# Performance work log

Hardware: AMD Instinct MI355X
Metric: run time of the kernel (lower is better)

## Reference

```python
import jax, jax.numpy as jnp
import numpy as np

IMG, P, C = 224, 16, 3
D, H, MLP = 512, 8, 2048
L, NCLS = 10, 10      # budget, classes
N = (IMG // P) ** 2   # 196 patches
PD = C * P * P        # patch_dim = 768


def setup_inputs() -> dict:
    key = jax.random.key(0)
    ks = jax.random.split(key, 32)
    w = lambda k, shape: (jax.random.normal(k, shape, jnp.float32) * 0.02)
    return {
        'x': jax.random.normal(ks[0], (32, C, IMG, IMG), jnp.float32),
        'y': jax.random.randint(ks[1], (32, 1), 0, NCLS),
        'pos_emb': w(ks[2], (1, N + 1, D)),
        'cls_tok': w(ks[3], (1, 1, D)),
        'Wp': w(ks[4], (D, PD)), 'bp': jnp.zeros((D,), jnp.float32),
        'Wqkv': w(ks[5], (3 * D, D)),
        'Wo': w(ks[6], (D, D)), 'bo': jnp.zeros((D,), jnp.float32),
        'ln1_g': jnp.ones((D,), jnp.float32), 'ln1_b': jnp.zeros((D,), jnp.float32),
        'ln2_g': jnp.ones((D,), jnp.float32), 'ln2_b': jnp.zeros((D,), jnp.float32),
        'W1': w(ks[7], (MLP, D)), 'b1': jnp.zeros((MLP,), jnp.float32),
        'W2': w(ks[8], (D, MLP)), 'b2': jnp.zeros((D,), jnp.float32),
        'lnh_g': jnp.ones((D,), jnp.float32), 'lnh_b': jnp.zeros((D,), jnp.float32),
        'Wh1': w(ks[9], (MLP, D)), 'bh1': jnp.zeros((MLP,), jnp.float32),
        'Wh2': w(ks[10], (1, MLP)), 'bh2': jnp.zeros((1,), jnp.float32),
        'lnc_g': jnp.ones((D,), jnp.float32), 'lnc_b': jnp.zeros((D,), jnp.float32),
        'Wc1': w(ks[11], (MLP, D)), 'bc1': jnp.zeros((MLP,), jnp.float32),
        'Wc2': w(ks[12], (NCLS, MLP)), 'bc2': jnp.zeros((NCLS,), jnp.float32),
    }


def _ln(u, g, b):
    mu = u.mean(-1, keepdims=True)
    v = ((u - mu) ** 2).mean(-1, keepdims=True)
    return (u - mu) / jnp.sqrt(v + 1e-5) * g + b


def _gelu(u):
    return jax.nn.gelu(u, approximate=False)


def reference(x, y, pos_emb, cls_tok, Wp, bp, Wqkv, Wo, bo,
              ln1_g, ln1_b, ln2_g, ln2_b, W1, b1, W2, b2,
              lnh_g, lnh_b, Wh1, bh1, Wh2, bh2,
              lnc_g, lnc_b, Wc1, bc1, Wc2, bc2):
    b = x.shape[0]
    hp = IMG // P
    # patchify: b c (h p1) (w p2) -> b (h w) (p1 p2 c)
    xp = x.reshape(b, C, hp, P, hp, P).transpose(0, 2, 4, 3, 5, 1).reshape(b, N, PD)
    e = xp @ Wp.T + bp                                   # [b, N, D]
    z = jnp.concatenate([jnp.broadcast_to(cls_tok, (b, 1, D)), e], 1) + pos_emb[:, :N + 1]

    scale = D ** -0.5

    def attn(u):
        q, k, v = jnp.split(u @ Wqkv.T, 3, axis=-1)
        hsplit = lambda t: t.reshape(b, -1, H, D // H).transpose(0, 2, 1, 3)  # b h n d
        q, k, v = hsplit(q), hsplit(k), hsplit(v)
        a = jax.nn.softmax(jnp.einsum('bhid,bhjd->bhij', q, k) * scale, axis=-1)
        o = jnp.einsum('bhij,bhjd->bhid', a, v).transpose(0, 2, 1, 3).reshape(b, -1, D)
        return o @ Wo.T + bo

    def ff(u):
        return _gelu(u @ W1.T + b1) @ W2.T + b2

    def halt(u):
        h = _gelu(_ln(u, lnh_g, lnh_b) @ Wh1.T + bh1) @ Wh2.T + bh2  # [b, n, 1]
        return jax.nn.sigmoid(h).mean(1)[:, 0]                        # [b]

    def step(u, _):
        u = u + attn(_ln(u, ln1_g, ln1_b))
        u = u + ff(_ln(u, ln2_g, ln2_b))
        return u, (u[:, 0], halt(u))

    _, (cls_outs, halts) = jax.lax.scan(step, z, None, length=L)
    cls_outs = cls_outs.transpose(1, 0, 2)   # [b, L, D]
    halts = halts.T                          # [b, L]

    logits = _gelu(_ln(cls_outs, lnc_g, lnc_b) @ Wc1.T + bc1) @ Wc2.T + bc2  # [b, L, 10]
    logp = jax.nn.log_softmax(logits, -1)
    lab = y[:, 0]
    ce = -jnp.take_along_axis(logp, jnp.broadcast_to(lab[:, None, None], (b, L, 1)), axis=2)[..., 0]  # [b, L]

    idx = jnp.argmin(ce, axis=1) + 1                     # [b], halting step per sample
    steps = jnp.arange(L)
    mask = (steps[None, :] < idx[:, None]).astype(ce.dtype)
    denom = idx.astype(ce.dtype)
    ref_ce = (ce * mask).sum(1) / denom                  # per-sample mean over first idx steps

    # halt labels: 1 for steps < idx-1, 0 at step idx-1 (only first idx entries count)
    hl = jnp.where(steps[None, :] == (idx[:, None] - 1), 0.0, 1.0)
    p = jnp.clip(halts, 1e-7, 1.0 - 1e-7)
    bce = -(hl * jnp.log(p) + (1.0 - hl) * jnp.log1p(-p))
    halt_loss = (bce * mask).sum(1) / denom

    return ref_ce.mean() + halt_loss.mean()
```

## Files before the change

### kernel.cpp

```cpp
#include <hip/hip_runtime.h>
#include <math.h>

#define BBATCH 32
#define NTOK 197
#define NPATCH 196
#define PDIM 768
#define DDIM 512
#define NHEAD 8
#define DHEAD 64
#define MLPDIM 2048
#define NLAYER 10
#define NCLASS 10
#define MTOK (BBATCH*NTOK)
#define MPAD 6400
#define MPATCH (BBATCH*NPATCH)
#define QKVROWS (MTOK + 16)

typedef unsigned short u16;
typedef __attribute__((ext_vector_type(8))) short bf16x8;
typedef __attribute__((ext_vector_type(4))) float f32x4;
typedef __attribute__((ext_vector_type(8))) unsigned short ushort8;

__device__ __forceinline__ float gelu_f(float x) {
    return 0.5f * x * (1.0f + erff(x * 0.70710678118654752440f));
}
__device__ __forceinline__ float bf2f(u16 u) {
    union { unsigned int i; float f; } v; v.i = ((unsigned int)u) << 16; return v.f;
}
__device__ __forceinline__ u16 f2bf(float f) {
    union { float f; unsigned int u; } v; v.f = f;
    unsigned int r = v.u + 0x7FFFu + ((v.u >> 16) & 1u);
    return (u16)(r >> 16);
}
__device__ __forceinline__ void gload_lds16(const u16* g, u16* l) {
    __builtin_amdgcn_global_load_lds((const __attribute__((address_space(1))) void*)g,
                                     (__attribute__((address_space(3))) void*)l, 16, 0, 0);
}

template<int ACT, int HASB, int HASR, int OUTBF, int HALT>
__global__ __launch_bounds__(256)
void mgemm_kernel(const u16* __restrict__ A, const u16* __restrict__ W,
                  const float* __restrict__ bias, const float* __restrict__ res,
                  void* __restrict__ Cout, int M, int Nn, int K)
{
    __shared__ u16 As[2][128 * 64];
    __shared__ u16 Bs[2][128 * 64];
    const int tid = threadIdx.x;
    const int lane = tid & 63;
    const int wid = tid >> 6;
    const int wr = wid >> 1, wc = wid & 1;

    const int gx = gridDim.x;
    const int nwg = gx * gridDim.y;
    const int wg = blockIdx.y * gx + blockIdx.x;
    const int q = nwg >> 3, r = nwg & 7;
    const int xcd = wg & 7, idx = wg >> 3;
    const int swz = (xcd < r) ? xcd * (q + 1) + idx
                              : r * (q + 1) + (xcd - r) * q + idx;
    const int m0 = (swz / gx) * 128, n0 = (swz % gx) * 128;

    f32x4 acc[4][4] = {};

    const int srow = tid >> 3;
    const int dcb  = (tid & 7) << 4;

    auto stage = [&](int buf, int k0) {
        #pragma unroll
        for (int p = 0; p < 4; ++p) {
            int rr = p * 32 + srow;
            int scb = dcb ^ ((rr & 7) << 4);
            gload_lds16(A + (size_t)(m0 + rr) * K + k0 + (scb >> 1), &As[buf][p * 2048 + tid * 8]);
            gload_lds16(W + (size_t)(n0 + rr) * K + k0 + (scb >> 1), &Bs[buf][p * 2048 + tid * 8]);
        }
    };
    auto compute = [&](int buf) {
        #pragma unroll
        for (int kk = 0; kk < 64; kk += 32) {
            const int kb = (kk + ((lane >> 4) << 3)) << 1;
            bf16x8 af[4], bfr[4];
            #pragma unroll
            for (int mi = 0; mi < 4; ++mi) {
                int ar = wr * 64 + mi * 16 + (lane & 15);
                af[mi] = *(const bf16x8*)&As[buf][ar * 64 + ((kb ^ ((ar & 7) << 4)) >> 1)];
            }
            #pragma unroll
            for (int ni = 0; ni < 4; ++ni) {
                int br = wc * 64 + ni * 16 + (lane & 15);
                bfr[ni] = *(const bf16x8*)&Bs[buf][br * 64 + ((kb ^ ((br & 7) << 4)) >> 1)];
            }
            #pragma unroll
            for (int mi = 0; mi < 4; ++mi)
                #pragma unroll
                for (int ni = 0; ni < 4; ++ni)
                    acc[mi][ni] = __builtin_amdgcn_mfma_f32_16x16x32_bf16(
                        af[mi], bfr[ni], acc[mi][ni], 0, 0, 0);
        }
    };

    const int NT = K >> 6;
    stage(0, 0);
    int cur = 0;
    #pragma unroll 1
    for (int t = 0; t < NT - 1; ++t) {
        stage(cur ^ 1, (t + 1) << 6);
        asm volatile("s_waitcnt vmcnt(8)" ::: "memory");
        __builtin_amdgcn_s_barrier();
        compute(cur);
        __builtin_amdgcn_s_barrier();
        cur ^= 1;
    }
    asm volatile("s_waitcnt vmcnt(0)" ::: "memory");
    __builtin_amdgcn_s_barrier();
    compute(cur);

    if (HALT) {
        const float* Wh2v = res;
        float* hout = (float*)Cout;
        #pragma unroll
        for (int mi = 0; mi < 4; ++mi) {
            #pragma unroll
            for (int j = 0; j < 4; ++j) {
                int row = m0 + wr * 64 + mi * 16 + ((lane >> 4) << 2) + j;
                float part = 0.0f;
                #pragma unroll
                for (int ni = 0; ni < 4; ++ni) {
                    int col = n0 + wc * 64 + ni * 16 + (lane & 15);
                    float v = gelu_f(acc[mi][ni][j] + bias[col]);
                    part += v * Wh2v[col];
                }
                #pragma unroll
                for (int off = 1; off < 16; off <<= 1) part += __shfl_xor(part, off, 64);
                if ((lane & 15) == 0 && row < M) atomicAdd(&hout[row], part);
            }
        }
        return;
    }

    float* outf = (float*)Cout;
    u16*   outb = (u16*)Cout;
    #pragma unroll
    for (int mi = 0; mi < 4; ++mi) {
        #pragma unroll
        for (int j = 0; j < 4; ++j) {
            int row = m0 + wr * 64 + mi * 16 + ((lane >> 4) << 2) + j;
            if (row >= M) continue;
            #pragma unroll
            for (int ni = 0; ni < 4; ++ni) {
                int col = n0 + wc * 64 + ni * 16 + (lane & 15);
                float v = acc[mi][ni][j];
                if (HASB) v += bias[col];
                if (ACT)  v = gelu_f(v);
                if (HASR) v += res[(size_t)row * Nn + col];
                if (OUTBF) outb[(size_t)row * Nn + col] = f2bf(v);
                else       outf[(size_t)row * Nn + col] = v;
            }
        }
    }
}

__global__ __launch_bounds__(256)
void f2bf_kernel(const float* __restrict__ in, u16* __restrict__ out, int n4)
{
    int i = blockIdx.x * 256 + threadIdx.x;
    if (i >= n4) return;
    float4 v = ((const float4*)in)[i];
    u16 o0 = f2bf(v.x), o1 = f2bf(v.y), o2 = f2bf(v.z), o3 = f2bf(v.w);
    out[i * 4 + 0] = o0; out[i * 4 + 1] = o1; out[i * 4 + 2] = o2; out[i * 4 + 3] = o3;
}

__global__ __launch_bounds__(256)
void ln_kernel(const float* __restrict__ X, const float* __restrict__ g,
               const float* __restrict__ bb, u16* __restrict__ Y, int M)
{
    int wave = (blockIdx.x * 4) + (threadIdx.x >> 6);
    int lane = threadIdx.x & 63;
    if (wave >= M) return;
    const float* x = X + (size_t)wave * DDIM;
    float v[8];
    float s = 0.0f;
    #pragma unroll
    for (int i = 0; i < 8; i++) { v[i] = x[lane + i * 64]; s += v[i]; }
    #pragma unroll
    for (int off = 32; off; off >>= 1) s += __shfl_xor(s, off, 64);
    float mu = s * (1.0f / 512.0f);
    float q = 0.0f;
    #pragma unroll
    for (int i = 0; i < 8; i++) { float d = v[i] - mu; q += d * d; }
    #pragma unroll
    for (int off = 32; off; off >>= 1) q += __shfl_xor(q, off, 64);
    float inv = 1.0f / sqrtf(q * (1.0f / 512.0f) + 1e-5f);
    u16* y = Y + (size_t)wave * DDIM;
    #pragma unroll
    for (int i = 0; i < 8; i++) {
        int c = lane + i * 64;
        y[c] = f2bf((v[i] - mu) * inv * g[c] + bb[c]);
    }
}

__global__ __launch_bounds__(256)
void patch_kernel(const float* __restrict__ x, u16* __restrict__ xp)
{
    size_t idx = (size_t)blockIdx.x * 256 + threadIdx.x;
    if (idx >= (size_t)MPATCH * PDIM) return;
    int pd = (int)(idx % PDIM);
    int bn = (int)(idx / PDIM);
    int n = bn % NPATCH, b = bn / NPATCH;
    int c = pd % 3, pix = pd / 3;
    int px = pix % 16, py = pix / 16;
    int hx = n % 14, hy = n / 14;
    int row = hy * 16 + py, col = hx * 16 + px;
    xp[idx] = f2bf(x[((size_t)(b * 3 + c) * 224 + row) * 224 + col]);
}

__global__ __launch_bounds__(256)
void assemble_kernel(const float* __restrict__ e, const float* __restrict__ clstok,
                     const float* __restrict__ pos, float* __restrict__ U)
{
    size_t idx = (size_t)blockIdx.x * 256 + threadIdx.x;
    if (idx >= (size_t)MTOK * DDIM) return;
    int d = (int)(idx % DDIM);
    int bt = (int)(idx / DDIM);
    int t = bt % NTOK, b = bt / NTOK;
    float v = (t == 0) ? clstok[d] : e[((size_t)b * NPATCH + (t - 1)) * DDIM + d];
    U[idx] = v + pos[t * DDIM + d];
}

__global__ __launch_bounds__(256)
void attn_mfma_kernel(const u16* __restrict__ qkv, u16* __restrict__ O)
{
    __shared__ u16 Ks[208 * 64];
    __shared__ u16 Vt[64 * 208];
    __shared__ u16 Pl[4 * 16 * 208];

    const int bh = blockIdx.x >> 1;
    const int half = blockIdx.x & 1;
    const int b = bh >> 3, h = bh & 7;
    const int tid = threadIdx.x;
    const int lane = tid & 63, wid = tid >> 6;
    const size_t base = ((size_t)b * NTOK) * 1536 + (size_t)h * 64;

    {
        int j0 = tid >> 3;
        int d0 = (tid & 7) * 8;
        for (int p = 0; p < 7; ++p) {
            int j = p * 32 + j0;
            if (j < 208) {
                bf16x8 v = {};
                if (j < NTOK) v = *(const bf16x8*)&qkv[base + (size_t)j * 1536 + 512 + d0];
                int byt = (j * 128 + d0 * 2) ^ ((j & 7) << 4);
                *(bf16x8*)((char*)Ks + byt) = v;
            }
        }
    }
    {
        int d = tid & 63;
        int jg = tid >> 6;
        for (int j = jg * 52; j < jg * 52 + 52; ++j) {
            u16 v = (j < NTOK) ? qkv[base + (size_t)j * 1536 + 1024 + d] : (u16)0;
            int byt = (d * 416 + j * 2) ^ ((d & 7) << 4);
            *(u16*)((char*)Vt + byt) = v;
        }
    }
    __syncthreads();

    u16* Pw = Pl + wid * 16 * 208;
    const float scale = 0.04419417382415922f;
    const int t0   = half ? 7 : 0;
    const int tcnt = half ? 6 : 7;
    const int g = lane >> 4;
    const int mycol = lane & 15;

    for (int ti = wid; ti < tcnt; ti += 4) {
        const int r0 = (t0 + ti) * 16;
        bf16x8 qf[2];
        #pragma unroll
        for (int ks = 0; ks < 2; ++ks) {
            int row = r0 + mycol;
            int col = ks * 32 + (g << 3);
            qf[ks] = *(const bf16x8*)&qkv[base + (size_t)row * 1536 + col];
        }
        f32x4 s[13];
        #pragma unroll
        for (int ct = 0; ct < 13; ++ct) s[ct] = (f32x4){0.f, 0.f, 0.f, 0.f};
        #pragma unroll
        for (int ks = 0; ks < 2; ++ks) {
            int kbyte = (ks * 32 + (g << 3)) * 2;
            #pragma unroll
            for (int ct = 0; ct < 13; ++ct) {
                int n = ct * 16 + mycol;
                bf16x8 kf = *(const bf16x8*)((char*)Ks + ((n * 128 + kbyte) ^ ((n & 7) << 4)));
                s[ct] = __builtin_amdgcn_mfma_f32_16x16x32_bf16(qf[ks], kf, s[ct], 0, 0, 0);
            }
        }
        float m[4], sum[4];
        #pragma unroll
        for (int j = 0; j < 4; ++j) m[j] = -1e30f;
        #pragma unroll
        for (int ct = 0; ct < 13; ++ct) {
            bool valid = (ct * 16 + mycol) < NTOK;
            #pragma unroll
            for (int j = 0; j < 4; ++j) {
                float v = valid ? s[ct][j] * scale : -1e30f;
                s[ct][j] = v;
                m[j] = fmaxf(m[j], v);
            }
        }
        #pragma unroll
        for (int off = 1; off < 16; off <<= 1)
            #pragma unroll
            for (int j = 0; j < 4; ++j) m[j] = fmaxf(m[j], __shfl_xor(m[j], off, 64));
        #pragma unroll
        for (int j = 0; j < 4; ++j) sum[j] = 0.0f;
        #pragma unroll
        for (int ct = 0; ct < 13; ++ct)
            #pragma unroll
            for (int j = 0; j < 4; ++j) {
                float e = expf(s[ct][j] - m[j]);
                s[ct][j] = e;
                sum[j] += e;
            }
        #pragma unroll
        for (int off = 1; off < 16; off <<= 1)
            #pragma unroll
            for (int j = 0; j < 4; ++j) sum[j] += __shfl_xor(sum[j], off, 64);
        float inv[4];
        #pragma unroll
        for (int j = 0; j < 4; ++j) inv[j] = 1.0f / sum[j];
        #pragma unroll
        for (int ct = 0; ct < 13; ++ct) {
            int col = ct * 16 + mycol;
            #pragma unroll
            for (int j = 0; j < 4; ++j) {
                int row = (g << 2) + j;
                int byt = (row * 416 + col * 2) ^ ((row & 7) << 4);
                *(u16*)((char*)Pw + byt) = f2bf(s[ct][j] * inv[j]);
            }
        }
        #pragma unroll
        for (int nt = 0; nt < 4; ++nt) {
            f32x4 o = (f32x4){0.f, 0.f, 0.f, 0.f};
            #pragma unroll
            for (int ks = 0; ks < 7; ++ks) {
                bf16x8 pf = {}, vf = {};
                bool live = !(ks == 6 && g >= 2);
                if (live) {
                    int kbyte = (ks * 32 + (g << 3)) * 2;
                    pf = *(const bf16x8*)((char*)Pw + ((mycol * 416 + kbyte) ^ ((mycol & 7) << 4)));
                    int vrow = nt * 16 + mycol;
                    vf = *(const bf16x8*)((char*)Vt + ((vrow * 416 + kbyte) ^ ((vrow & 7) << 4)));
                }
                o = __builtin_amdgcn_mfma_f32_16x16x32_bf16(pf, vf, o, 0, 0, 0);
            }
            #pragma unroll
            for (int j = 0; j < 4; ++j) {
                int grow = r0 + (g << 2) + j;
                if (grow < NTOK)
                    O[((size_t)b * NTOK + grow) * DDIM + h * 64 + nt * 16 + mycol] = f2bf(o[j]);
            }
        }
    }
}

__global__ __launch_bounds__(64)
void halt_mean_cls_kernel(const float* __restrict__ hsc, const float* __restrict__ bh2,
                          const float* __restrict__ U,
                          float* __restrict__ halts, float* __restrict__ cls, int l)
{
    int b = blockIdx.x, lane = threadIdx.x;
    float bb = bh2[0];
    float s = 0.0f;
    for (int t = lane; t < NTOK; t += 64) {
        float raw = hsc[b * NTOK + t] + bb;
        s += 1.0f / (1.0f + expf(-raw));
    }
    #pragma unroll
    for (int off = 32; off; off >>= 1) s += __shfl_xor(s, off, 64);
    if (lane == 0) halts[b * NLAYER + l] = s * (1.0f / (float)NTOK);
    for (int d = lane; d < DDIM; d += 64)
        cls[((size_t)b * NLAYER + l) * DDIM + d] = U[(size_t)b * NTOK * DDIM + d];
}

__global__ __launch_bounds__(256)
void head_logits_kernel(const u16* __restrict__ Hh, const float* __restrict__ Wc2,
                        const float* __restrict__ bc2, float* __restrict__ logits)
{
    int wave = (blockIdx.x * 4) + (threadIdx.x >> 6);
    int lane = threadIdx.x & 63;
    if (wave >= BBATCH * NLAYER) return;
    const u16* row = Hh + (size_t)wave * MLPDIM;
    float rv[32];
    #pragma unroll
    for (int i = 0; i < 32; i++) rv[i] = bf2f(row[lane + i * 64]);
    #pragma unroll
    for (int c = 0; c < NCLASS; c++) {
        float s = 0.0f;
        #pragma unroll
        for (int i = 0; i < 32; i++) s = fmaf(rv[i], Wc2[c * MLPDIM + lane + i * 64], s);
        #pragma unroll
        for (int off = 32; off; off >>= 1) s += __shfl_xor(s, off, 64);
        if (lane == 0) logits[wave * NCLASS + c] = s + bc2[c];
    }
}

__global__ __launch_bounds__(256)
void ce_kernel(const float* __restrict__ logits, const int* __restrict__ y,
               float* __restrict__ ce)
{
    int r = blockIdx.x * 256 + threadIdx.x;
    if (r >= BBATCH * NLAYER) return;
    const float* lg = logits + (size_t)r * NCLASS;
    float mx = lg[0];
    #pragma unroll
    for (int i = 1; i < NCLASS; i++) mx = fmaxf(mx, lg[i]);
    float s = 0.0f;
    #pragma unroll
    for (int i = 0; i < NCLASS; i++) s += expf(lg[i] - mx);
    int lab = y[r / NLAYER];
    ce[r] = -(lg[lab] - mx - logf(s));
}

__global__ __launch_bounds__(64)
void loss_kernel(const float* __restrict__ ce, const float* __restrict__ halts,
                 float* __restrict__ out)
{
    int b = threadIdx.x;
    float total = 0.0f;
    if (b < BBATCH) {
        const float* c = ce + b * NLAYER;
        int idx = 0; float mn = c[0];
        for (int l = 1; l < NLAYER; l++) if (c[l] < mn) { mn = c[l]; idx = l; }
        idx += 1;
        float acc = 0.0f;
        for (int l = 0; l < idx; l++) {
            acc += c[l];
            float p = halts[b * NLAYER + l];
            p = fminf(fmaxf(p, 1e-7f), 1.0f - 1e-7f);
            float hl = (l == idx - 1) ? 0.0f : 1.0f;
            acc += -(hl * logf(p) + (1.0f - hl) * log1pf(-p));
        }
        total = acc / (float)idx;
    }
    #pragma unroll
    for (int off = 32; off; off >>= 1) total += __shfl_xor(total, off, 64);
    if (threadIdx.x == 0) out[0] = total * (1.0f / (float)BBATCH);
}

extern "C" void kernel_launch(void* const* d_in, const int* in_sizes, int n_in,
                              void* d_out, int out_size, void* d_ws, size_t ws_size,
                              hipStream_t stream)
{
    const float* x      = (const float*)d_in[0];
    const int*   y      = (const int*)d_in[1];
    const float* pos    = (const float*)d_in[2];
    const float* clstok = (const float*)d_in[3];
    const float* Wp     = (const float*)d_in[4];
    const float* bp     = (const float*)d_in[5];
    const float* Wqkv   = (const float*)d_in[6];
    const float* Wo     = (const float*)d_in[7];
    const float* bo     = (const float*)d_in[8];
    const float* ln1g   = (const float*)d_in[9];
    const float* ln1b   = (const float*)d_in[10];
    const float* ln2g   = (const float*)d_in[11];
    const float* ln2b   = (const float*)d_in[12];
    const float* W1     = (const float*)d_in[13];
    const float* b1     = (const float*)d_in[14];
    const float* W2     = (const float*)d_in[15];
    const float* b2     = (const float*)d_in[16];
    const float* lnhg   = (const float*)d_in[17];
    const float* lnhb   = (const float*)d_in[18];
    const float* Wh1    = (const float*)d_in[19];
    const float* bh1    = (const float*)d_in[20];
    const float* Wh2    = (const float*)d_in[21];
    const float* bh2    = (const float*)d_in[22];
    const float* lncg   = (const float*)d_in[23];
    const float* lncb   = (const float*)d_in[24];
    const float* Wc1    = (const float*)d_in[25];
    const float* bc1    = (const float*)d_in[26];
    const float* Wc2    = (const float*)d_in[27];
    const float* bc2    = (const float*)d_in[28];

    float* U      = (float*)d_ws;
    float* EMB    = U + (size_t)MTOK * DDIM;
    float* CLS    = EMB + (size_t)MPATCH * DDIM;
    float* LOGITS = CLS + (size_t)BBATCH * NLAYER * DDIM;
    float* CE     = LOGITS + BBATCH * NLAYER * NCLASS;
    float* HSC    = CE + BBATCH * NLAYER;
    float* HALTS  = HSC + MTOK;
    u16* QKVb = (u16*)(HALTS + BBATCH * NLAYER + 32);
    u16* LNB  = QKVb + (size_t)QKVROWS * 1536;
    u16* HB   = LNB + (size_t)MPAD * DDIM;
    u16* XP   = HB + (size_t)MPAD * MLPDIM;
    u16* CLNB = XP + (size_t)MPATCH * PDIM;
    u16* wWp  = CLNB + 384 * DDIM;
    u16* wWqkv= wWp   + 512 * 768;
    u16* wWo  = wWqkv + 1536 * 512;
    u16* wW1  = wWo   + 512 * 512;
    u16* wW2  = wW1   + 2048 * 512;
    u16* wWh1 = wW2   + 512 * 2048;
    u16* wWc1 = wWh1  + 2048 * 512;

    dim3 blk(256);

    f2bf_kernel<<<dim3((512*768/4 + 255)/256), blk, 0, stream>>>(Wp, wWp, 512*768/4);
    f2bf_kernel<<<dim3((1536*512/4 + 255)/256), blk, 0, stream>>>(Wqkv, wWqkv, 1536*512/4);
    f2bf_kernel<<<dim3((512*512/4 + 255)/256), blk, 0, stream>>>(Wo, wWo, 512*512/4);
    f2bf_kernel<<<dim3((2048*512/4 + 255)/256), blk, 0, stream>>>(W1, wW1, 2048*512/4);
    f2bf_kernel<<<dim3((512*2048/4 + 255)/256), blk, 0, stream>>>(W2, wW2, 512*2048/4);
    f2bf_kernel<<<dim3((2048*512/4 + 255)/256), blk, 0, stream>>>(Wh1, wWh1, 2048*512/4);
    f2bf_kernel<<<dim3((2048*512/4 + 255)/256), blk, 0, stream>>>(Wc1, wWc1, 2048*512/4);

    patch_kernel<<<dim3(((size_t)MPATCH * PDIM + 255) / 256), blk, 0, stream>>>(x, XP);
    mgemm_kernel<0,1,0,0,0><<<dim3(DDIM/128, MPATCH/128), blk, 0, stream>>>(
        XP, wWp, bp, nullptr, (void*)EMB, MPATCH, DDIM, PDIM);
    assemble_kernel<<<dim3(((size_t)MTOK * DDIM + 255) / 256), blk, 0, stream>>>(
        EMB, clstok, pos, U);

    const int MT = (MTOK + 127) / 128;

    for (int l = 0; l < NLAYER; l++) {
        ln_kernel<<<dim3((MTOK + 3) / 4), blk, 0, stream>>>(U, ln1g, ln1b, LNB, MTOK);
        mgemm_kernel<0,0,0,1,0><<<dim3(1536/128, MT), blk, 0, stream>>>(
            LNB, wWqkv, nullptr, nullptr, (void*)QKVb, MTOK, 1536, DDIM);
        attn_mfma_kernel<<<dim3(512), blk, 0, stream>>>(QKVb, LNB);
        mgemm_kernel<0,1,1,0,0><<<dim3(DDIM/128, MT), blk, 0, stream>>>(
            LNB, wWo, bo, U, (void*)U, MTOK, DDIM, DDIM);
        ln_kernel<<<dim3((MTOK + 3) / 4), blk, 0, stream>>>(U, ln2g, ln2b, LNB, MTOK);
        mgemm_kernel<1,1,0,1,0><<<dim3(MLPDIM/128, MT), blk, 0, stream>>>(
            LNB, wW1, b1, nullptr, (void*)HB, MTOK, MLPDIM, DDIM);
        mgemm_kernel<0,1,1,0,0><<<dim3(DDIM/128, MT), blk, 0, stream>>>(
            HB, wW2, b2, U, (void*)U, MTOK, DDIM, MLPDIM);
        ln_kernel<<<dim3((MTOK + 3) / 4), blk, 0, stream>>>(U, lnhg, lnhb, LNB, MTOK);
        hipMemsetAsync(HSC, 0, MTOK * sizeof(float), stream);
        mgemm_kernel<0,1,0,0,1><<<dim3(MLPDIM/128, MT), blk, 0, stream>>>(
            LNB, wWh1, bh1, Wh2, (void*)HSC, MTOK, MLPDIM, DDIM);
        halt_mean_cls_kernel<<<dim3(BBATCH), dim3(64), 0, stream>>>(
            HSC, bh2, U, HALTS, CLS, l);
    }

    ln_kernel<<<dim3((BBATCH * NLAYER + 3) / 4), blk, 0, stream>>>(
        CLS, lncg, lncb, CLNB, BBATCH * NLAYER);
    mgemm_kernel<1,1,0,1,0><<<dim3(MLPDIM/128, 3), blk, 0, stream>>>(
        CLNB, wWc1, bc1, nullptr, (void*)HB, BBATCH * NLAYER, MLPDIM, DDIM);
    head_logits_kernel<<<dim3((BBATCH * NLAYER + 3) / 4), blk, 0, stream>>>(
        HB, Wc2, bc2, LOGITS);
    ce_kernel<<<dim3(2), blk, 0, stream>>>(LOGITS, y, CE);
    loss_kernel<<<dim3(1), dim3(64), 0, stream>>>(CE, HALTS, (float*)d_out);
}
```

Baseline: 2.276 ms.

## Restructure ViT pipeline: fused dual LN, co-scheduled QKV/halt GEMMs, split-K W2

```diff
diff --git a/kernel.cpp b/kernel.cpp
--- a/kernel.cpp
+++ b/kernel.cpp
@@ -19,7 +19,6 @@
 typedef unsigned short u16;
 typedef __attribute__((ext_vector_type(8))) short bf16x8;
 typedef __attribute__((ext_vector_type(4))) float f32x4;
-typedef __attribute__((ext_vector_type(8))) unsigned short ushort8;
 
 __device__ __forceinline__ float gelu_f(float x) {
     return 0.5f * x * (1.0f + erff(x * 0.70710678118654752440f));
@@ -36,41 +35,53 @@
     __builtin_amdgcn_global_load_lds((const __attribute__((address_space(1))) void*)g,
                                      (__attribute__((address_space(3))) void*)l, 16, 0, 0);
 }
-
-template<int ACT, int HASB, int HASR, int OUTBF, int HALT>
-__global__ __launch_bounds__(256)
-void mgemm_kernel(const u16* __restrict__ A, const u16* __restrict__ W,
-                  const float* __restrict__ bias, const float* __restrict__ res,
-                  void* __restrict__ Cout, int M, int Nn, int K)
-{
-    __shared__ u16 As[2][128 * 64];
+__device__ __forceinline__ int swz_bij(int wg, int nwg) {
+    int q = nwg >> 3, r = nwg & 7, xcd = wg & 7, id8 = wg >> 3;
+    return (xcd < r) ? xcd * (q + 1) + id8 : r * (q + 1) + (xcd - r) * q + id8;
+}
+
+template<int MODEA, int MODEB>
+__global__ __launch_bounds__(512)
+void gemm256_kernel(int nA, int colsA, int colsB,
+                    const u16* __restrict__ Aa, const u16* __restrict__ Wa,
+                    const float* __restrict__ biasa, void* __restrict__ outa, int Na,
+                    const u16* __restrict__ Ab, const u16* __restrict__ Wb,
+                    const float* __restrict__ biasb, const float* __restrict__ wh2,
+                    void* __restrict__ outb, int Nb, int M)
+{
+    __shared__ u16 As[2][256 * 64];
     __shared__ u16 Bs[2][128 * 64];
-    const int tid = threadIdx.x;
-    const int lane = tid & 63;
-    const int wid = tid >> 6;
+    const int tid = threadIdx.x, lane = tid & 63, wid = tid >> 6;
     const int wr = wid >> 1, wc = wid & 1;
 
-    const int gx = gridDim.x;
-    const int nwg = gx * gridDim.y;
-    const int wg = blockIdx.y * gx + blockIdx.x;
-    const int q = nwg >> 3, r = nwg & 7;
-    const int xcd = wg & 7, idx = wg >> 3;
-    const int swz = (xcd < r) ? xcd * (q + 1) + idx
-                              : r * (q + 1) + (xcd - r) * q + idx;
-    const int m0 = (swz / gx) * 128, n0 = (swz % gx) * 128;
+    const int swz = swz_bij(blockIdx.x, gridDim.x);
+    int mode, m0, n0, Nn;
+    const u16 *A, *W; const float* bias; void* out;
+    if (swz < nA) {
+        mode = MODEA; A = Aa; W = Wa; bias = biasa; out = outa; Nn = Na;
+        m0 = (swz / colsA) * 256; n0 = (swz % colsA) * 128;
+    } else {
+        int s2 = swz - nA;
+        mode = MODEB; A = Ab; W = Wb; bias = biasb; out = outb; Nn = Nb;
+        m0 = (s2 / colsB) * 256; n0 = (s2 % colsB) * 128;
+    }
 
     f32x4 acc[4][4] = {};
-
     const int srow = tid >> 3;
     const int dcb  = (tid & 7) << 4;
 
     auto stage = [&](int buf, int k0) {
         #pragma unroll
         for (int p = 0; p < 4; ++p) {
-            int rr = p * 32 + srow;
+            int rr = p * 64 + srow;
             int scb = dcb ^ ((rr & 7) << 4);
-            gload_lds16(A + (size_t)(m0 + rr) * K + k0 + (scb >> 1), &As[buf][p * 2048 + tid * 8]);
-            gload_lds16(W + (size_t)(n0 + rr) * K + k0 + (scb >> 1), &Bs[buf][p * 2048 + tid * 8]);
+            gload_lds16(A + (size_t)(m0 + rr) * 512 + k0 + (scb >> 1), &As[buf][p * 4096 + tid * 8]);
+        }
+        #pragma unroll
+        for (int p = 0; p < 2; ++p) {
+            int rr = p * 64 + srow;
+            int scb = dcb ^ ((rr & 7) << 4);
+            gload_lds16(W + (size_t)(n0 + rr) * 512 + k0 + (scb >> 1), &Bs[buf][p * 4096 + tid * 8]);
         }
     };
     auto compute = [&](int buf) {
@@ -97,13 +108,12 @@
         }
     };
 
-    const int NT = K >> 6;
     stage(0, 0);
     int cur = 0;
     #pragma unroll 1
-    for (int t = 0; t < NT - 1; ++t) {
+    for (int t = 0; t < 7; ++t) {
         stage(cur ^ 1, (t + 1) << 6);
-        asm volatile("s_waitcnt vmcnt(8)" ::: "memory");
+        asm volatile("s_waitcnt vmcnt(6)" ::: "memory");
         __builtin_amdgcn_s_barrier();
         compute(cur);
         __builtin_amdgcn_s_barrier();
@@ -113,9 +123,8 @@
     __builtin_amdgcn_s_barrier();
     compute(cur);
 
-    if (HALT) {
-        const float* Wh2v = res;
-        float* hout = (float*)Cout;
+    if (mode == 1) {
+        float* hout = (float*)out;
         #pragma unroll
         for (int mi = 0; mi < 4; ++mi) {
             #pragma unroll
@@ -125,8 +134,7 @@
                 #pragma unroll
                 for (int ni = 0; ni < 4; ++ni) {
                     int col = n0 + wc * 64 + ni * 16 + (lane & 15);
-                    float v = gelu_f(acc[mi][ni][j] + bias[col]);
-                    part += v * Wh2v[col];
+                    part += gelu_f(acc[mi][ni][j] + bias[col]) * wh2[col];
                 }
                 #pragma unroll
                 for (int off = 1; off < 16; off <<= 1) part += __shfl_xor(part, off, 64);
@@ -135,6 +143,94 @@
         }
         return;
     }
+    u16* outb16 = (u16*)out;
+    #pragma unroll
+    for (int mi = 0; mi < 4; ++mi) {
+        #pragma unroll
+        for (int j = 0; j < 4; ++j) {
+            int row = m0 + wr * 64 + mi * 16 + ((lane >> 4) << 2) + j;
+            if (row >= M) continue;
+            #pragma unroll
+            for (int ni = 0; ni < 4; ++ni) {
+                int col = n0 + wc * 64 + ni * 16 + (lane & 15);
+                float v = acc[mi][ni][j];
+                if (mode == 2) v = gelu_f(v + bias[col]);
+                outb16[(size_t)row * Nn + col] = f2bf(v);
+            }
+        }
+    }
+}
+
+template<int ACT, int HASB, int HASR, int OUTBF, int ATOMIC>
+__global__ __launch_bounds__(256)
+void mgemm_kernel(const u16* __restrict__ A, const u16* __restrict__ W,
+                  const float* __restrict__ bias, const float* __restrict__ res,
+                  void* __restrict__ Cout, int M, int Nn, int K, int kcount, int mtiles)
+{
+    __shared__ u16 As[2][128 * 64];
+    __shared__ u16 Bs[2][128 * 64];
+    const int tid = threadIdx.x, lane = tid & 63, wid = tid >> 6;
+    const int wr = wid >> 1, wc = wid & 1;
+
+    const int gx = gridDim.x;
+    const int swz = swz_bij(blockIdx.y * gx + blockIdx.x, gx * gridDim.y);
+    const int ry = swz / gx;
+    const int ks = ry / mtiles;
+    const int m0 = (ry % mtiles) * 128, n0 = (swz % gx) * 128;
+    const int kbase = ks * kcount;
+
+    f32x4 acc[4][4] = {};
+    const int srow = tid >> 3;
+    const int dcb  = (tid & 7) << 4;
+
+    auto stage = [&](int buf, int k0) {
+        #pragma unroll
+        for (int p = 0; p < 4; ++p) {
+            int rr = p * 32 + srow;
+            int scb = dcb ^ ((rr & 7) << 4);
+            gload_lds16(A + (size_t)(m0 + rr) * K + k0 + (scb >> 1), &As[buf][p * 2048 + tid * 8]);
+            gload_lds16(W + (size_t)(n0 + rr) * K + k0 + (scb >> 1), &Bs[buf][p * 2048 + tid * 8]);
+        }
+    };
+    auto compute = [&](int buf) {
+        #pragma unroll
+        for (int kk = 0; kk < 64; kk += 32) {
+            const int kb = (kk + ((lane >> 4) << 3)) << 1;
+            bf16x8 af[4], bfr[4];
+            #pragma unroll
+            for (int mi = 0; mi < 4; ++mi) {
+                int ar = wr * 64 + mi * 16 + (lane & 15);
+                af[mi] = *(const bf16x8*)&As[buf][ar * 64 + ((kb ^ ((ar & 7) << 4)) >> 1)];
+            }
+            #pragma unroll
+            for (int ni = 0; ni < 4; ++ni) {
+                int br = wc * 64 + ni * 16 + (lane & 15);
+                bfr[ni] = *(const bf16x8*)&Bs[buf][br * 64 + ((kb ^ ((br & 7) << 4)) >> 1)];
+            }
+            #pragma unroll
+            for (int mi = 0; mi < 4; ++mi)
+                #pragma unroll
+                for (int ni = 0; ni < 4; ++ni)
+                    acc[mi][ni] = __builtin_amdgcn_mfma_f32_16x16x32_bf16(
+                        af[mi], bfr[ni], acc[mi][ni], 0, 0, 0);
+        }
+    };
+
+    const int NT = kcount >> 6;
+    stage(0, kbase);
+    int cur = 0;
+    #pragma unroll 1
+    for (int t = 0; t < NT - 1; ++t) {
+        stage(cur ^ 1, kbase + ((t + 1) << 6));
+        asm volatile("s_waitcnt vmcnt(8)" ::: "memory");
+        __builtin_amdgcn_s_barrier();
+        compute(cur);
+        __builtin_amdgcn_s_barrier();
+        cur ^= 1;
+    }
+    asm volatile("s_waitcnt vmcnt(0)" ::: "memory");
+    __builtin_amdgcn_s_barrier();
+    compute(cur);
 
     float* outf = (float*)Cout;
     u16*   outb = (u16*)Cout;
@@ -148,89 +244,164 @@
             for (int ni = 0; ni < 4; ++ni) {
                 int col = n0 + wc * 64 + ni * 16 + (lane & 15);
                 float v = acc[mi][ni][j];
-                if (HASB) v += bias[col];
-                if (ACT)  v = gelu_f(v);
-                if (HASR) v += res[(size_t)row * Nn + col];
-                if (OUTBF) outb[(size_t)row * Nn + col] = f2bf(v);
-                else       outf[(size_t)row * Nn + col] = v;
-            }
-        }
-    }
-}
-
-__global__ __launch_bounds__(256)
-void f2bf_kernel(const float* __restrict__ in, u16* __restrict__ out, int n4)
-{
-    int i = blockIdx.x * 256 + threadIdx.x;
-    if (i >= n4) return;
-    float4 v = ((const float4*)in)[i];
-    u16 o0 = f2bf(v.x), o1 = f2bf(v.y), o2 = f2bf(v.z), o3 = f2bf(v.w);
-    out[i * 4 + 0] = o0; out[i * 4 + 1] = o1; out[i * 4 + 2] = o2; out[i * 4 + 3] = o3;
-}
-
-__global__ __launch_bounds__(256)
-void ln_kernel(const float* __restrict__ X, const float* __restrict__ g,
-               const float* __restrict__ bb, u16* __restrict__ Y, int M)
-{
-    int wave = (blockIdx.x * 4) + (threadIdx.x >> 6);
+                if (ATOMIC) {
+                    if (HASB && ks == 0) v += bias[col];
+                    atomicAdd(&outf[(size_t)row * Nn + col], v);
+                } else {
+                    if (HASB) v += bias[col];
+                    if (ACT)  v = gelu_f(v);
+                    if (HASR) v += res[(size_t)row * Nn + col];
+                    if (OUTBF) outb[(size_t)row * Nn + col] = f2bf(v);
+                    else       outf[(size_t)row * Nn + col] = v;
+                }
+            }
+        }
+    }
+}
+
+__global__ __launch_bounds__(256)
+void ln_one_kernel(const float* __restrict__ X, const float* __restrict__ g,
+                   const float* __restrict__ bb, u16* __restrict__ Y, int M)
+{
+    int w0 = blockIdx.x * 4 + (threadIdx.x >> 6);
     int lane = threadIdx.x & 63;
-    if (wave >= M) return;
-    const float* x = X + (size_t)wave * DDIM;
-    float v[8];
-    float s = 0.0f;
-    #pragma unroll
-    for (int i = 0; i < 8; i++) { v[i] = x[lane + i * 64]; s += v[i]; }
-    #pragma unroll
-    for (int off = 32; off; off >>= 1) s += __shfl_xor(s, off, 64);
-    float mu = s * (1.0f / 512.0f);
-    float q = 0.0f;
-    #pragma unroll
-    for (int i = 0; i < 8; i++) { float d = v[i] - mu; q += d * d; }
-    #pragma unroll
-    for (int off = 32; off; off >>= 1) q += __shfl_xor(q, off, 64);
-    float inv = 1.0f / sqrtf(q * (1.0f / 512.0f) + 1e-5f);
-    u16* y = Y + (size_t)wave * DDIM;
-    #pragma unroll
-    for (int i = 0; i < 8; i++) {
-        int c = lane + i * 64;
-        y[c] = f2bf((v[i] - mu) * inv * g[c] + bb[c]);
+    int stride = gridDim.x * 4;
+    for (int row = w0; row < M; row += stride) {
+        const float* x = X + (size_t)row * DDIM;
+        float v[8], s = 0.0f;
+        #pragma unroll
+        for (int i = 0; i < 8; i++) { v[i] = x[lane + i * 64]; s += v[i]; }
+        #pragma unroll
+        for (int off = 32; off; off >>= 1) s += __shfl_xor(s, off, 64);
+        float mu = s * (1.0f / 512.0f), q = 0.0f;
+        #pragma unroll
+        for (int i = 0; i < 8; i++) { float d = v[i] - mu; q += d * d; }
+        #pragma unroll
+        for (int off = 32; off; off >>= 1) q += __shfl_xor(q, off, 64);
+        float inv = 1.0f / sqrtf(q * (1.0f / 512.0f) + 1e-5f);
+        u16* y = Y + (size_t)row * DDIM;
+        #pragma unroll
+        for (int i = 0; i < 8; i++) {
+            int c = lane + i * 64;
+            y[c] = f2bf((v[i] - mu) * inv * g[c] + bb[c]);
+        }
+    }
+}
+
+__global__ __launch_bounds__(256)
+void ln_dual_kernel(const float* __restrict__ X,
+                    const float* __restrict__ g1, const float* __restrict__ b1,
+                    const float* __restrict__ g2, const float* __restrict__ b2,
+                    u16* __restrict__ Y1, u16* __restrict__ Y2, int M)
+{
+    int w0 = blockIdx.x * 4 + (threadIdx.x >> 6);
+    int lane = threadIdx.x & 63;
+    int stride = gridDim.x * 4;
+    for (int row = w0; row < M; row += stride) {
+        const float* x = X + (size_t)row * DDIM;
+        float v[8], s = 0.0f;
+        #pragma unroll
+        for (int i = 0; i < 8; i++) { v[i] = x[lane + i * 64]; s += v[i]; }
+        #pragma unroll
+        for (int off = 32; off; off >>= 1) s += __shfl_xor(s, off, 64);
+        float mu = s * (1.0f / 512.0f), q = 0.0f;
+        #pragma unroll
+        for (int i = 0; i < 8; i++) { float d = v[i] - mu; q += d * d; }
+        #pragma unroll
+        for (int off = 32; off; off >>= 1) q += __shfl_xor(q, off, 64);
+        float inv = 1.0f / sqrtf(q * (1.0f / 512.0f) + 1e-5f);
+        u16* y1 = Y1 + (size_t)row * DDIM;
+        u16* y2 = Y2 + (size_t)row * DDIM;
+        #pragma unroll
+        for (int i = 0; i < 8; i++) {
+            int c = lane + i * 64;
+            float n = (v[i] - mu) * inv;
+            y1[c] = f2bf(n * g1[c] + b1[c]);
+            y2[c] = f2bf(n * g2[c] + b2[c]);
+        }
     }
 }
 
 __global__ __launch_bounds__(256)
 void patch_kernel(const float* __restrict__ x, u16* __restrict__ xp)
 {
-    size_t idx = (size_t)blockIdx.x * 256 + threadIdx.x;
-    if (idx >= (size_t)MPATCH * PDIM) return;
-    int pd = (int)(idx % PDIM);
-    int bn = (int)(idx / PDIM);
-    int n = bn % NPATCH, b = bn / NPATCH;
-    int c = pd % 3, pix = pd / 3;
-    int px = pix % 16, py = pix / 16;
-    int hx = n % 14, hy = n / 14;
-    int row = hy * 16 + py, col = hx * 16 + px;
-    xp[idx] = f2bf(x[((size_t)(b * 3 + c) * 224 + row) * 224 + col]);
+    const size_t total = (size_t)MPATCH * PDIM;
+    for (size_t idx = (size_t)blockIdx.x * 256 + threadIdx.x; idx < total;
+         idx += (size_t)gridDim.x * 256) {
+        int pd = (int)(idx % PDIM);
+        int bn = (int)(idx / PDIM);
+        int n = bn % NPATCH, b = bn / NPATCH;
+        int c = pd % 3, pix = pd / 3;
+        int px = pix % 16, py = pix / 16;
+        int hx = n % 14, hy = n / 14;
+        int row = hy * 16 + py, col = hx * 16 + px;
+        xp[idx] = f2bf(x[((size_t)(b * 3 + c) * 224 + row) * 224 + col]);
+    }
 }
 
 __global__ __launch_bounds__(256)
 void assemble_kernel(const float* __restrict__ e, const float* __restrict__ clstok,
                      const float* __restrict__ pos, float* __restrict__ U)
 {
-    size_t idx = (size_t)blockIdx.x * 256 + threadIdx.x;
-    if (idx >= (size_t)MTOK * DDIM) return;
-    int d = (int)(idx % DDIM);
-    int bt = (int)(idx / DDIM);
-    int t = bt % NTOK, b = bt / NTOK;
-    float v = (t == 0) ? clstok[d] : e[((size_t)b * NPATCH + (t - 1)) * DDIM + d];
-    U[idx] = v + pos[t * DDIM + d];
-}
-
-__global__ __launch_bounds__(256)
-void attn_mfma_kernel(const u16* __restrict__ qkv, u16* __restrict__ O)
+    const size_t total = (size_t)MTOK * DDIM;
+    for (size_t idx = (size_t)blockIdx.x * 256 + threadIdx.x; idx < total;
+         idx += (size_t)gridDim.x * 256) {
+        int d = (int)(idx % DDIM);
+        int bt = (int)(idx / DDIM);
+        int t = bt % NTOK, b = bt / NTOK;
+        float v = (t == 0) ? clstok[d] : e[((size_t)b * NPATCH + (t - 1)) * DDIM + d];
+        U[idx] = v + pos[t * DDIM + d];
+    }
+}
+
+__global__ __launch_bounds__(256)
+void convert7_kernel(const float* s0, const float* s1, const float* s2,
+                     const float* s3, const float* s4, const float* s5,
+                     const float* s6, u16* __restrict__ dst)
+{
+    const int total4 = 1409024;
+    for (int i4 = blockIdx.x * 256 + threadIdx.x; i4 < total4; i4 += gridDim.x * 256) {
+        size_t e = (size_t)i4 * 4;
+        const float* s; size_t off;
+        if      (e < 393216)  { s = s0; off = 0; }
+        else if (e < 1179648) { s = s1; off = 393216; }
+        else if (e < 1441792) { s = s2; off = 1179648; }
+        else if (e < 2490368) { s = s3; off = 1441792; }
+        else if (e < 3538944) { s = s4; off = 2490368; }
+        else if (e < 4587520) { s = s5; off = 3538944; }
+        else                  { s = s6; off = 4587520; }
+        float4 v = ((const float4*)s)[(e - off) >> 2];
+        dst[e + 0] = f2bf(v.x); dst[e + 1] = f2bf(v.y);
+        dst[e + 2] = f2bf(v.z); dst[e + 3] = f2bf(v.w);
+    }
+}
+
+template<int HM>
+__global__ __launch_bounds__(256)
+void attn_hm_kernel(const u16* __restrict__ qkv, u16* __restrict__ O,
+                    const float* __restrict__ hsc, const float* __restrict__ bh2,
+                    const float* __restrict__ U, float* __restrict__ halts,
+                    float* __restrict__ cls, int lidx)
 {
     __shared__ u16 Ks[208 * 64];
     __shared__ u16 Vt[64 * 208];
     __shared__ u16 Pl[4 * 16 * 208];
+
+    if (HM && blockIdx.x >= 512) {
+        int b = blockIdx.x - 512;
+        int ln = threadIdx.x;
+        if (ln >= 64) return;
+        float bb = bh2[0];
+        float s = 0.0f;
+        for (int t = ln; t < NTOK; t += 64)
+            s += 1.0f / (1.0f + expf(-(hsc[b * NTOK + t] + bb)));
+        #pragma unroll
+        for (int off = 32; off; off >>= 1) s += __shfl_xor(s, off, 64);
+        if (ln == 0) halts[b * NLAYER + lidx] = s * (1.0f / (float)NTOK);
+        for (int d = ln; d < DDIM; d += 64)
+            cls[((size_t)b * NLAYER + lidx) * DDIM + d] = U[(size_t)b * NTOK * DDIM + d];
+        return;
+    }
 
     const int bh = blockIdx.x >> 1;
     const int half = blockIdx.x & 1;
@@ -362,22 +533,20 @@
 }
 
 __global__ __launch_bounds__(64)
-void halt_mean_cls_kernel(const float* __restrict__ hsc, const float* __restrict__ bh2,
-                          const float* __restrict__ U,
-                          float* __restrict__ halts, float* __restrict__ cls, int l)
+void haltmean_kernel(const float* __restrict__ hsc, const float* __restrict__ bh2,
+                     const float* __restrict__ U, float* __restrict__ halts,
+                     float* __restrict__ cls, int lidx)
 {
     int b = blockIdx.x, lane = threadIdx.x;
     float bb = bh2[0];
     float s = 0.0f;
-    for (int t = lane; t < NTOK; t += 64) {
-        float raw = hsc[b * NTOK + t] + bb;
-        s += 1.0f / (1.0f + expf(-raw));
-    }
+    for (int t = lane; t < NTOK; t += 64)
+        s += 1.0f / (1.0f + expf(-(hsc[b * NTOK + t] + bb)));
     #pragma unroll
     for (int off = 32; off; off >>= 1) s += __shfl_xor(s, off, 64);
-    if (lane == 0) halts[b * NLAYER + l] = s * (1.0f / (float)NTOK);
+    if (lane == 0) halts[b * NLAYER + lidx] = s * (1.0f / (float)NTOK);
     for (int d = lane; d < DDIM; d += 64)
-        cls[((size_t)b * NLAYER + l) * DDIM + d] = U[(size_t)b * NTOK * DDIM + d];
+        cls[((size_t)b * NLAYER + lidx) * DDIM + d] = U[(size_t)b * NTOK * DDIM + d];
 }
 
 __global__ __launch_bounds__(256)
@@ -403,46 +572,45 @@
 }
 
 __global__ __launch_bounds__(256)
-void ce_kernel(const float* __restrict__ logits, const int* __restrict__ y,
-               float* __restrict__ ce)
-{
-    int r = blockIdx.x * 256 + threadIdx.x;
-    if (r >= BBATCH * NLAYER) return;
-    const float* lg = logits + (size_t)r * NCLASS;
-    float mx = lg[0];
-    #pragma unroll
-    for (int i = 1; i < NCLASS; i++) mx = fmaxf(mx, lg[i]);
-    float s = 0.0f;
-    #pragma unroll
-    for (int i = 0; i < NCLASS; i++) s += expf(lg[i] - mx);
-    int lab = y[r / NLAYER];
-    ce[r] = -(lg[lab] - mx - logf(s));
-}
-
-__global__ __launch_bounds__(64)
-void loss_kernel(const float* __restrict__ ce, const float* __restrict__ halts,
-                 float* __restrict__ out)
-{
-    int b = threadIdx.x;
-    float total = 0.0f;
-    if (b < BBATCH) {
-        const float* c = ce + b * NLAYER;
+void celoss_kernel(const float* __restrict__ logits, const int* __restrict__ y,
+                   const float* __restrict__ halts, float* __restrict__ out)
+{
+    __shared__ float ceS[BBATCH * NLAYER];
+    __shared__ float bl[BBATCH];
+    int tid = threadIdx.x;
+    for (int r = tid; r < BBATCH * NLAYER; r += 256) {
+        const float* lg = logits + (size_t)r * NCLASS;
+        float mx = lg[0];
+        #pragma unroll
+        for (int i = 1; i < NCLASS; i++) mx = fmaxf(mx, lg[i]);
+        float s = 0.0f;
+        #pragma unroll
+        for (int i = 0; i < NCLASS; i++) s += expf(lg[i] - mx);
+        int lab = y[r / NLAYER];
+        ceS[r] = -(lg[lab] - mx - logf(s));
+    }
+    __syncthreads();
+    if (tid < BBATCH) {
+        const float* c = ceS + tid * NLAYER;
         int idx = 0; float mn = c[0];
         for (int l = 1; l < NLAYER; l++) if (c[l] < mn) { mn = c[l]; idx = l; }
         idx += 1;
         float acc = 0.0f;
         for (int l = 0; l < idx; l++) {
             acc += c[l];
-            float p = halts[b * NLAYER + l];
+            float p = halts[tid * NLAYER + l];
             p = fminf(fmaxf(p, 1e-7f), 1.0f - 1e-7f);
             float hl = (l == idx - 1) ? 0.0f : 1.0f;
             acc += -(hl * logf(p) + (1.0f - hl) * log1pf(-p));
         }
-        total = acc / (float)idx;
-    }
-    #pragma unroll
-    for (int off = 32; off; off >>= 1) total += __shfl_xor(total, off, 64);
-    if (threadIdx.x == 0) out[0] = total * (1.0f / (float)BBATCH);
+        bl[tid] = acc / (float)idx;
+    }
+    __syncthreads();
+    if (tid == 0) {
+        float t = 0.0f;
+        for (int b = 0; b < BBATCH; b++) t += bl[b];
+        out[0] = t * (1.0f / (float)BBATCH);
+    }
 }
 
 extern "C" void kernel_launch(void* const* d_in, const int* in_sizes, int n_in,
@@ -480,17 +648,18 @@
     const float* bc2    = (const float*)d_in[28];
 
     float* U      = (float*)d_ws;
-    float* EMB    = U + (size_t)MTOK * DDIM;
-    float* CLS    = EMB + (size_t)MPATCH * DDIM;
+    float* CLS    = U + (size_t)MTOK * DDIM;
     float* LOGITS = CLS + (size_t)BBATCH * NLAYER * DDIM;
-    float* CE     = LOGITS + BBATCH * NLAYER * NCLASS;
-    float* HSC    = CE + BBATCH * NLAYER;
-    float* HALTS  = HSC + MTOK;
+    float* HSC    = LOGITS + BBATCH * NLAYER * NCLASS;
+    float* HALTS  = HSC + (size_t)NLAYER * MTOK;
     u16* QKVb = (u16*)(HALTS + BBATCH * NLAYER + 32);
-    u16* LNB  = QKVb + (size_t)QKVROWS * 1536;
-    u16* HB   = LNB + (size_t)MPAD * DDIM;
-    u16* XP   = HB + (size_t)MPAD * MLPDIM;
-    u16* CLNB = XP + (size_t)MPATCH * PDIM;
+    float* EMB = (float*)QKVb;
+    u16* LNB1 = QKVb + (size_t)QKVROWS * 1536;
+    u16* LNB2 = LNB1 + (size_t)MPAD * DDIM;
+    u16* LNBh = LNB2 + (size_t)MPAD * DDIM;
+    u16* HB   = LNBh + (size_t)MPAD * DDIM;
+    u16* XP   = HB;
+    u16* CLNB = HB + (size_t)MPAD * MLPDIM;
     u16* wWp  = CLNB + 384 * DDIM;
     u16* wWqkv= wWp   + 512 * 768;
     u16* wWo  = wWqkv + 1536 * 512;
@@ -500,49 +669,54 @@
     u16* wWc1 = wWh1  + 2048 * 512;
 
     dim3 blk(256);
-
-    f2bf_kernel<<<dim3((512*768/4 + 255)/256), blk, 0, stream>>>(Wp, wWp, 512*768/4);
-    f2bf_kernel<<<dim3((1536*512/4 + 255)/256), blk, 0, stream>>>(Wqkv, wWqkv, 1536*512/4);
-    f2bf_kernel<<<dim3((512*512/4 + 255)/256), blk, 0, stream>>>(Wo, wWo, 512*512/4);
-    f2bf_kernel<<<dim3((2048*512/4 + 255)/256), blk, 0, stream>>>(W1, wW1, 2048*512/4);
-    f2bf_kernel<<<dim3((512*2048/4 + 255)/256), blk, 0, stream>>>(W2, wW2, 512*2048/4);
-    f2bf_kernel<<<dim3((2048*512/4 + 255)/256), blk, 0, stream>>>(Wh1, wWh1, 2048*512/4);
-    f2bf_kernel<<<dim3((2048*512/4 + 255)/256), blk, 0, stream>>>(Wc1, wWc1, 2048*512/4);
-
-    patch_kernel<<<dim3(((size_t)MPATCH * PDIM + 255) / 256), blk, 0, stream>>>(x, XP);
-    mgemm_kernel<0,1,0,0,0><<<dim3(DDIM/128, MPATCH/128), blk, 0, stream>>>(
-        XP, wWp, bp, nullptr, (void*)EMB, MPATCH, DDIM, PDIM);
-    assemble_kernel<<<dim3(((size_t)MTOK * DDIM + 255) / 256), blk, 0, stream>>>(
-        EMB, clstok, pos, U);
-
-    const int MT = (MTOK + 127) / 128;
+    const u16* dummyA = LNB1; const float* dummyF = bh2;
+
+    convert7_kernel<<<dim3(1024), blk, 0, stream>>>(Wp, Wqkv, Wo, W1, W2, Wh1, Wc1, wWp);
+    hipMemsetAsync(HSC, 0, (size_t)NLAYER * MTOK * sizeof(float), stream);
+    patch_kernel<<<dim3(2048), blk, 0, stream>>>(x, XP);
+    mgemm_kernel<0,1,0,0,0><<<dim3(4, 49), blk, 0, stream>>>(
+        XP, wWp, bp, nullptr, (void*)EMB, MPATCH, DDIM, PDIM, PDIM, 49);
+    assemble_kernel<<<dim3(2048), blk, 0, stream>>>(EMB, clstok, pos, U);
+    ln_dual_kernel<<<dim3(256), blk, 0, stream>>>(U, ln1g, ln1b, lnhg, lnhb, LNB1, LNBh, MTOK);
 
     for (int l = 0; l < NLAYER; l++) {
-        ln_kernel<<<dim3((MTOK + 3) / 4), blk, 0, stream>>>(U, ln1g, ln1b, LNB, MTOK);
-        mgemm_kernel<0,0,0,1,0><<<dim3(1536/128, MT), blk, 0, stream>>>(
-            LNB, wWqkv, nullptr, nullptr, (void*)QKVb, MTOK, 1536, DDIM);
-        attn_mfma_kernel<<<dim3(512), blk, 0, stream>>>(QKVb, LNB);
-        mgemm_kernel<0,1,1,0,0><<<dim3(DDIM/128, MT), blk, 0, stream>>>(
-            LNB, wWo, bo, U, (void*)U, MTOK, DDIM, DDIM);
-        ln_kernel<<<dim3((MTOK + 3) / 4), blk, 0, stream>>>(U, ln2g, ln2b, LNB, MTOK);
-        mgemm_kernel<1,1,0,1,0><<<dim3(MLPDIM/128, MT), blk, 0, stream>>>(
-            LNB, wW1, b1, nullptr, (void*)HB, MTOK, MLPDIM, DDIM);
-        mgemm_kernel<0,1,1,0,0><<<dim3(DDIM/128, MT), blk, 0, stream>>>(
-            HB, wW2, b2, U, (void*)U, MTOK, DDIM, MLPDIM);
-        ln_kernel<<<dim3((MTOK + 3) / 4), blk, 0, stream>>>(U, lnhg, lnhb, LNB, MTOK);
-        hipMemsetAsync(HSC, 0, MTOK * sizeof(float), stream);
-        mgemm_kernel<0,1,0,0,1><<<dim3(MLPDIM/128, MT), blk, 0, stream>>>(
-            LNB, wWh1, bh1, Wh2, (void*)HSC, MTOK, MLPDIM, DDIM);
-        halt_mean_cls_kernel<<<dim3(BBATCH), dim3(64), 0, stream>>>(
-            HSC, bh2, U, HALTS, CLS, l);
-    }
-
-    ln_kernel<<<dim3((BBATCH * NLAYER + 3) / 4), blk, 0, stream>>>(
-        CLS, lncg, lncb, CLNB, BBATCH * NLAYER);
-    mgemm_kernel<1,1,0,1,0><<<dim3(MLPDIM/128, 3), blk, 0, stream>>>(
-        CLNB, wWc1, bc1, nullptr, (void*)HB, BBATCH * NLAYER, MLPDIM, DDIM);
-    head_logits_kernel<<<dim3((BBATCH * NLAYER + 3) / 4), blk, 0, stream>>>(
-        HB, Wc2, bc2, LOGITS);
-    ce_kernel<<<dim3(2), blk, 0, stream>>>(LOGITS, y, CE);
-    loss_kernel<<<dim3(1), dim3(64), 0, stream>>>(CE, HALTS, (float*)d_out);
-}
+        if (l == 0) {
+            gemm256_kernel<0,0><<<dim3(300), dim3(512), 0, stream>>>(
+                300, 12, 12, LNB1, wWqkv, nullptr, (void*)QKVb, 1536,
+                LNB1, wWqkv, nullptr, nullptr, (void*)QKVb, 1536, MTOK);
+        } else {
+            gemm256_kernel<0,1><<<dim3(700), dim3(512), 0, stream>>>(
+                300, 12, 16, LNB1, wWqkv, nullptr, (void*)QKVb, 1536,
+                LNBh, wWh1, bh1, Wh2, (void*)(HSC + (size_t)(l-1) * MTOK), 2048, MTOK);
+        }
+        if (l == 0) {
+            attn_hm_kernel<0><<<dim3(512), blk, 0, stream>>>(
+                QKVb, LNB1, nullptr, dummyF, U, HALTS, CLS, 0);
+        } else {
+            attn_hm_kernel<1><<<dim3(544), blk, 0, stream>>>(
+                QKVb, LNB1, HSC + (size_t)(l-1) * MTOK, bh2, U, HALTS, CLS, l - 1);
+        }
+        mgemm_kernel<0,1,1,0,0><<<dim3(4, 50), blk, 0, stream>>>(
+            LNB1, wWo, bo, U, (void*)U, MTOK, DDIM, DDIM, DDIM, 50);
+        ln_one_kernel<<<dim3(256), blk, 0, stream>>>(U, ln2g, ln2b, LNB2, MTOK);
+        gemm256_kernel<2,2><<<dim3(400), dim3(512), 0, stream>>>(
+            400, 16, 16, LNB2, wW1, b1, (void*)HB, 2048,
+            LNB2, wW1, b1, nullptr, (void*)HB, 2048, MTOK);
+        mgemm_kernel<0,1,0,0,1><<<dim3(4, 100), blk, 0, stream>>>(
+            HB, wW2, b2, nullptr, (void*)U, MTOK, DDIM, MLPDIM, 1024, 50);
+        ln_dual_kernel<<<dim3(256), blk, 0, stream>>>(
+            U, ln1g, ln1b, lnhg, lnhb, LNB1, LNBh, MTOK);
+    }
+
+    gemm256_kernel<1,1><<<dim3(400), dim3(512), 0, stream>>>(
+        400, 16, 16, LNBh, wWh1, bh1, (void*)(HSC + (size_t)9 * MTOK), 2048,
+        LNBh, wWh1, bh1, Wh2, (void*)(HSC + (size_t)9 * MTOK), 2048, MTOK);
+    haltmean_kernel<<<dim3(BBATCH), dim3(64), 0, stream>>>(
+        HSC + (size_t)9 * MTOK, bh2, U, HALTS, CLS, 9);
+
+    ln_one_kernel<<<dim3(80), blk, 0, stream>>>(CLS, lncg, lncb, CLNB, BBATCH * NLAYER);
+    mgemm_kernel<1,1,0,1,0><<<dim3(16, 3), blk, 0, stream>>>(
+        CLNB, wWc1, bc1, nullptr, (void*)HB, BBATCH * NLAYER, MLPDIM, DDIM, DDIM, 3);
+    head_logits_kernel<<<dim3(80), blk, 0, stream>>>(HB, Wc2, bc2, LOGITS);
+    celoss_kernel<<<dim3(1), blk, 0, stream>>>(LOGITS, y, HALTS, (float*)d_out);
+}
```

Measured after the change: 2.251 ms. No clear change (-1.1%).
